# Kernel optimization log

Measured on AMD Instinct MI355X. Metric: run time of the kernel, lower is better.

Reference implementation:

```python
import jax, jax.numpy as jnp
import numpy as np

N_NODES = 100000
N_EDGES = 3200000
N_GRAPHS = 1000


def gcn_conv(x, row, col, norm, W, b, num_nodes):
    # x: [N, F_in] -> [N, F_out]; PyG GCNConv: linear, then normalized scatter-add
    h = x @ W                                   # [N, F_out]
    msg = norm[:, None] * h[row]                # gather from source nodes
    out = jax.ops.segment_sum(msg, col, num_segments=num_nodes)  # scatter to targets
    return out + b


def gcn_norm(edge_index, edge_weight, num_nodes):
    # add self-loops with weight 1.0 (PyG default, improved=False)
    loops = jnp.arange(num_nodes, dtype=edge_index.dtype)
    row = jnp.concatenate([edge_index[0], loops])
    col = jnp.concatenate([edge_index[1], loops])
    w = jnp.concatenate([edge_weight, jnp.ones(num_nodes, edge_weight.dtype)])
    deg = jax.ops.segment_sum(w, col, num_segments=num_nodes)
    dinv = jnp.where(deg > 0, jax.lax.rsqrt(jnp.maximum(deg, 1e-30)), 0.0)
    norm = dinv[row] * w * dinv[col]
    return row, col, norm


def setup_inputs() -> dict:
    key = jax.random.key(0)
    ks = jax.random.split(key, 8)
    x = jax.random.normal(ks[0], (N_NODES, 3), dtype=jnp.float32)
    edge_index = jax.random.randint(ks[1], (2, N_EDGES), 0, N_NODES, dtype=jnp.int64)
    edge_weight = jax.random.uniform(ks[2], (N_EDGES,), dtype=jnp.float32)
    batch = jnp.sort(jax.random.randint(ks[3], (N_NODES,), 0, N_GRAPHS, dtype=jnp.int64))
    W1 = jax.random.normal(ks[4], (3, 16), dtype=jnp.float32) * (1.0 / np.sqrt(3))
    b1 = jnp.zeros((16,), jnp.float32)
    W2 = jax.random.normal(ks[5], (16, 16), dtype=jnp.float32) * 0.25
    b2 = jnp.zeros((16,), jnp.float32)
    Wlin = jax.random.normal(ks[6], (16, 7), dtype=jnp.float32) * 0.25
    blin = jnp.zeros((7,), jnp.float32)
    return {"x": x, "edge_index": edge_index, "edge_weight": edge_weight,
            "batch": batch, "W1": W1, "b1": b1, "W2": W2, "b2": b2,
            "Wlin": Wlin, "blin": blin}


def reference(x, edge_index, edge_weight, batch, W1, b1, W2, b2, Wlin, blin):
    num_nodes = x.shape[0]
    row, col, norm = gcn_norm(edge_index, edge_weight, num_nodes)
    h = jax.nn.relu(gcn_conv(x, row, col, norm, W1, b1, num_nodes))
    h = jax.nn.relu(gcn_conv(h, row, col, norm, W2, b2, num_nodes))
    pooled = jax.ops.segment_sum(h, batch, num_segments=N_GRAPHS)  # [G, 16]
    return pooled @ Wlin + blin  # [G, 7]
```

## Files before the change

### kernel.cpp

```cpp
#include <hip/hip_runtime.h>


#define SH 6
#define RB 64
#define KMAX 2048
#define KST (KMAX + 1)
#define TPB 256
#define BCAP 8192
#define PT 1024
#define PB 256
#define NP 4
#define ETCAP 12800

typedef unsigned short ushort_t;
typedef unsigned char u8;
typedef unsigned long long u64;

__device__ __forceinline__ ushort_t f2bf(float v) {
    unsigned u = __float_as_uint(v);
    u += 0x7FFFu + ((u >> 16) & 1u);
    return (ushort_t)(u >> 16);
}

__device__ __forceinline__ unsigned quantw(float w) {
    unsigned wq = (unsigned)__float2int_rn(w * 32768.0f);
    return wq > 32767u ? 32767u : wq;
}

__global__ __launch_bounds__(PT)
void k_part(const int* __restrict__ row, const int* __restrict__ col,
            const float* __restrict__ ew, unsigned* __restrict__ bcnt,
            unsigned* __restrict__ bof, uint2* __restrict__ brc,
            int E, int K, int tile, int KP) {
    __shared__ unsigned lh[KMAX];
    __shared__ unsigned cur[KMAX];
    __shared__ unsigned wt[PT / 64];
    __shared__ unsigned lc[ETCAP];
    __shared__ unsigned lp[ETCAP];
    int tid = threadIdx.x, b = blockIdx.x;
    int e0 = min(b * tile, E), e1 = min(b * tile + tile, E);
    int cnt = e1 - e0;
    unsigned base = (unsigned)e0;
    bool staged = (cnt <= ETCAP);
    for (int i = tid; i < KMAX; i += PT) lh[i] = 0u;
    __syncthreads();
    if (staged) {
        for (int j = tid; j < cnt; j += PT) {
            int e = e0 + j;
            int c = col[e];
            lc[j] = (unsigned)c;
            lp[j] = (unsigned)row[e] | (quantw(ew[e]) << 17);
            atomicAdd(&lh[c >> SH], 1u);
        }
    } else {
        for (int e = e0 + tid; e < e1; e += PT) atomicAdd(&lh[col[e] >> SH], 1u);
    }
    __syncthreads();
    for (int i = tid; i < K; i += PT) {
        unsigned c = lh[i];
        if (c) atomicAdd(&bcnt[i], c);
    }
    int i0 = tid << 1;
    unsigned a0 = lh[i0], a1 = lh[i0 + 1];
    unsigned ts = a0 + a1, v = ts;
#pragma unroll
    for (int o = 1; o < 64; o <<= 1) {
        unsigned u = __shfl_up(v, o, 64);
        if ((tid & 63) >= o) v += u;
    }
    if ((tid & 63) == 63) wt[tid >> 6] = v;
    __syncthreads();
    if (tid == 0) {
        unsigned acc = 0;
#pragma unroll
        for (int w = 0; w < PT / 64; w++) { unsigned t = wt[w]; wt[w] = acc; acc += t; }
    }
    __syncthreads();
    unsigned ex = wt[tid >> 6] + (v - ts);
    unsigned* bo = bof + (size_t)b * KST;
    cur[i0] = base + ex;          bo[i0] = base + ex;
    cur[i0 + 1] = base + ex + a0; bo[i0 + 1] = base + ex + a0;
    if (tid == PT - 1) bo[KMAX] = base + ex + ts;
    __syncthreads();
    for (int p = 0; p < NP; ++p) {
        int lo = p * KP, hi = min(lo + KP, K);
        if (staged) {
            for (int j = tid; j < cnt; j += PT) {
                unsigned c = lc[j];
                int bkt = (int)(c >> SH);
                if (bkt >= lo && bkt < hi) {
                    unsigned pos = atomicAdd(&cur[bkt], 1u);
                    brc[pos] = make_uint2(lp[j], c);
                }
            }
        } else {
            for (int e = e0 + tid; e < e1; e += PT) {
                int c = col[e];
                int bkt = c >> SH;
                if (bkt >= lo && bkt < hi) {
                    unsigned pos = atomicAdd(&cur[bkt], 1u);
                    brc[pos] = make_uint2((unsigned)row[e] | (quantw(ew[e]) << 17),
                                          (unsigned)c);
                }
            }
        }
        __syncthreads();
    }
}

__global__ void k_scan(const unsigned* __restrict__ cnt, unsigned* __restrict__ start,
                       int K) {
    __shared__ unsigned a[KMAX], b[KMAX];
    int t = threadIdx.x;
    for (int i = t; i < KMAX; i += 1024) a[i] = (i < K) ? cnt[i] : 0u;
    __syncthreads();
    unsigned *src = a, *dst = b;
    for (int off = 1; off < KMAX; off <<= 1) {
        for (int i = t; i < KMAX; i += 1024)
            dst[i] = (i >= off) ? src[i] + src[i - off] : src[i];
        __syncthreads();
        unsigned* tmp = src; src = dst; dst = tmp;
    }
    for (int i = t; i < K; i += 1024) start[i] = (i == 0) ? 0u : src[i - 1];
}

__global__ __launch_bounds__(TPB)
void k_grp(const uint2* __restrict__ brc, const unsigned* __restrict__ bof,
           const unsigned* __restrict__ bst, const float* __restrict__ x,
           const float* __restrict__ W1, unsigned* __restrict__ srt,
           unsigned* __restrict__ cptr, float* __restrict__ dinv,
           unsigned* __restrict__ g1b, float* __restrict__ acc1,
           int N, int E, int K) {
    int orig = blockIdx.x;
    int q8 = K >> 3, r8 = K & 7;
    int xcd = orig & 7, idx = orig >> 3;
    int k = (xcd < r8 ? xcd * (q8 + 1) : r8 * (q8 + 1) + (xcd - r8) * q8) + idx;
    int node0 = k << SH;

    __shared__ unsigned ebuf[BCAP];
    __shared__ u8 cbuf[BCAP];
    __shared__ u8 seg[BCAP];
    __shared__ unsigned rsrc[PB];
    __shared__ unsigned roff[PB + 1];
    __shared__ unsigned wt4[TPB / 64];
    __shared__ unsigned cnt64[RB], st64[RB], dq[RB];
    __shared__ float dl[RB], lx[RB * 3], lw[48];
    int tid = threadIdx.x;
    unsigned s = bst[k];
    if (tid < RB) { cnt64[tid] = 0u; dq[tid] = 0u; }
    if (tid < 48) lw[tid] = W1[tid];
    int nn = min(RB, N - node0);
    for (int i = tid; i < nn * 3; i += TPB) lx[i] = x[(size_t)node0 * 3 + i];

    unsigned rl;
    {
        unsigned s0 = bof[(size_t)tid * KST + k];
        unsigned s1 = bof[(size_t)tid * KST + k + 1];
        rsrc[tid] = s0;
        rl = s1 - s0;
    }
    unsigned v = rl;
#pragma unroll
    for (int o = 1; o < 64; o <<= 1) {
        unsigned u = __shfl_up(v, o, 64);
        if ((tid & 63) >= o) v += u;
    }
    if ((tid & 63) == 63) wt4[tid >> 6] = v;
    __syncthreads();
    if (tid == 0) {
        unsigned acc = 0;
#pragma unroll
        for (int w = 0; w < TPB / 64; w++) { unsigned t = wt4[w]; wt4[w] = acc; acc += t; }
    }
    __syncthreads();
    unsigned ex = wt4[tid >> 6] + (v - rl);
    roff[tid] = ex;
    if (tid == PB - 1) roff[PB] = ex + rl;
    __syncthreads();
    unsigned c = roff[PB];

    bool fits = (c <= (unsigned)BCAP);
    if (fits) {
        for (unsigned j = ex; j < ex + rl; ++j) seg[j] = (u8)tid;
        __syncthreads();
        for (unsigned j = tid; j < c; j += TPB) {
            unsigned r = seg[j];
            unsigned src = rsrc[r] + (j - roff[r]);
            uint2 p = brc[src];
            unsigned cl = p.y & 63u;
            ebuf[j] = p.x; cbuf[j] = (u8)cl;
            atomicAdd(&cnt64[cl], 1u);
            atomicAdd(&dq[cl], p.x >> 17);
        }
        __syncthreads();
        if (tid == 0) {
            unsigned acc = 0;
            for (int i = 0; i < RB; i++) { st64[i] = acc; acc += cnt64[i]; cnt64[i] = 0u; }
        }
        __syncthreads();
        for (unsigned j = tid; j < c; j += TPB) {
            unsigned cl = cbuf[j];
            unsigned pos = st64[cl] + atomicAdd(&cnt64[cl], 1u);
            srt[s + pos] = ebuf[j];
        }
    } else {
#define MAP_SRC(j, srcv)                                                       \
        {                                                                      \
            int lo = 0, hi = PB - 1;                                           \
            _Pragma("unroll")                                                  \
            for (int it = 0; it < 8; ++it) {                                   \
                int mid = (lo + hi + 1) >> 1;                                  \
                if (roff[mid] <= (j)) lo = mid; else hi = mid - 1;             \
            }                                                                  \
            (srcv) = rsrc[lo] + ((j) - roff[lo]);                              \
        }
        for (unsigned j = tid; j < c; j += TPB) {
            unsigned src; MAP_SRC(j, src);
            uint2 p = brc[src];
            unsigned cl = p.y & 63u;
            atomicAdd(&cnt64[cl], 1u);
            atomicAdd(&dq[cl], p.x >> 17);
        }
        __syncthreads();
        if (tid == 0) {
            unsigned acc = 0;
            for (int i = 0; i < RB; i++) { st64[i] = acc; acc += cnt64[i]; cnt64[i] = 0u; }
        }
        __syncthreads();
        for (unsigned j = tid; j < c; j += TPB) {
            unsigned src; MAP_SRC(j, src);
            uint2 p = brc[src];
            unsigned cl = p.y & 63u;
            unsigned pos = st64[cl] + atomicAdd(&cnt64[cl], 1u);
            srt[s + pos] = p.x;
        }
#undef MAP_SRC
    }
    __syncthreads();
    if (tid < RB) {
        float d = rsqrtf(1.0f + (float)dq[tid] * (1.0f / 32768.0f));
        dl[tid] = d;
        if (tid < nn) {
            dinv[node0 + tid] = d;
            cptr[node0 + tid] = s + st64[tid];
        }
    }
    if (tid == 0 && node0 + nn == N) cptr[N] = (unsigned)E;
    __syncthreads();
    float* gtmp = (float*)ebuf;
    for (int idx2 = tid; idx2 < nn * 16; idx2 += TPB) {
        int n = idx2 >> 4, f = idx2 & 15;
        float vv = dl[n] * (lx[n * 3] * lw[f] + lx[n * 3 + 1] * lw[16 + f] +
                            lx[n * 3 + 2] * lw[32 + f]);
        acc1[(size_t)(node0 + n) * 16 + f] = vv;
        gtmp[idx2] = vv;
    }
    __syncthreads();
    for (int idx2 = tid; idx2 < nn * 8; idx2 += TPB) {
        int n = idx2 >> 3, qq = idx2 & 7;
        g1b[(size_t)(node0 + n) * 8 + qq] =
            (unsigned)f2bf(gtmp[n * 16 + 2 * qq]) |
            ((unsigned)f2bf(gtmp[n * 16 + 2 * qq + 1]) << 16);
    }
}

__global__ __launch_bounds__(TPB)
void k_csr(const unsigned* __restrict__ srt, const unsigned* __restrict__ cptr,
           const unsigned* __restrict__ gb, float* __restrict__ acc, int N) {
    int t = blockIdx.x * TPB + threadIdx.x;
    int c = t >> 3, f2 = t & 7;
    if (c >= N) return;
    unsigned e = cptr[c], end = cptr[c + 1];
    float a = 0.0f, b = 0.0f;
#pragma unroll 4
    for (; e < end; ++e) {
        unsigned m = srt[e];
        float w = (float)(m >> 17) * (1.0f / 32768.0f);
        unsigned u = gb[(size_t)(m & 0x1FFFFu) * 8 + f2];
        a = fmaf(w, __uint_as_float(u << 16), a);
        b = fmaf(w, __uint_as_float(u & 0xFFFF0000u), b);
    }
    float2* p = (float2*)&acc[(size_t)c * 16 + 2 * f2];
    float2 v = *p;
    v.x += a; v.y += b;
    *p = v;
}

__global__ void k_mid(const float* __restrict__ acc1, const float* __restrict__ dinv,
                      const float* __restrict__ b1, const float* __restrict__ W2,
                      unsigned* __restrict__ g2b, float* __restrict__ acc2, int N) {
    __shared__ float t[16][16];
    __shared__ float go[16][16];
    __shared__ float w2[256];
    int tid = threadIdx.x;
    int il = tid >> 4, f = tid & 15;
    int i = blockIdx.x * 16 + il;
    w2[tid] = W2[tid];
    float v = 0.0f, d = 0.0f;
    if (i < N) {
        d = dinv[i];
        v = b1[f] + d * acc1[(size_t)i * 16 + f];
        v = v > 0.0f ? v : 0.0f;
    }
    t[il][f] = v;
    __syncthreads();
    float r = 0.0f;
    if (i < N) {
        float o = 0.0f;
#pragma unroll
        for (int kk = 0; kk < 16; kk++) o += t[il][kk] * w2[kk * 16 + f];
        r = d * o;
        acc2[(size_t)i * 16 + f] = r;
    }
    go[il][f] = r;
    __syncthreads();
    if (tid < 128) {
        int il2 = tid >> 3, q = tid & 7;
        int i2 = blockIdx.x * 16 + il2;
        if (i2 < N)
            g2b[(size_t)i2 * 8 + q] = (unsigned)f2bf(go[il2][2 * q]) |
                                      ((unsigned)f2bf(go[il2][2 * q + 1]) << 16);
    }
}

#define PC 1024
__global__ void k_pool(const float* __restrict__ acc2, const float* __restrict__ dinv,
                       const float* __restrict__ b2, const int* __restrict__ batch,
                       float* __restrict__ pooled, int N, int G) {
    int b0 = blockIdx.x * PC;
    int nodes = min(PC, N - b0);
    __shared__ float lacc[64 * 16];
    __shared__ int lbat[PC];
    int tid = threadIdx.x;
    for (int i = tid; i < nodes; i += 256) lbat[i] = batch[b0 + i];
    __syncthreads();
    int gmin = lbat[0], gmax = lbat[nodes - 1];
    bool fits = (gmax - gmin < 64);
    if (fits) {
        for (int i = tid; i < 64 * 16; i += 256) lacc[i] = 0.0f;
        __syncthreads();
    }
    for (int idx = tid; idx < nodes * 16; idx += 256) {
        int i = idx >> 4, f = idx & 15;
        int n = b0 + i;
        float d = dinv[n];
        float v = b2[f] + d * acc2[(size_t)n * 16 + f];
        v = v > 0.0f ? v : 0.0f;
        if (fits) atomicAdd(&lacc[(lbat[i] - gmin) * 16 + f], v);
        else      atomicAdd(&pooled[lbat[i] * 16 + f], v);
    }
    if (fits) {
        __syncthreads();
        for (int idx = tid; idx < 64 * 16; idx += 256) {
            int g = gmin + (idx >> 4);
            float v = lacc[idx];
            if (g < G && v != 0.0f) atomicAdd(&pooled[g * 16 + (idx & 15)], v);
        }
    }
}

__global__ void k_final(const float* __restrict__ pooled, const float* __restrict__ Wlin,
                        const float* __restrict__ blin, float* __restrict__ out, int G) {
    int t = blockIdx.x * blockDim.x + threadIdx.x;
    int g = t / 7, j = t % 7;
    if (g >= G) return;
    float v = blin[j];
#pragma unroll
    for (int f = 0; f < 16; f++) v += pooled[g * 16 + f] * Wlin[f * 7 + j];
    out[g * 7 + j] = v;
}

static inline int cdiv_i(long long a, long long b) { return (int)((a + b - 1) / b); }

extern "C" void kernel_launch(void* const* d_in, const int* in_sizes, int n_in,
                              void* d_out, int out_size, void* d_ws, size_t ws_size,
                              hipStream_t stream) {
    const float* x     = (const float*)d_in[0];
    const int*   ei    = (const int*)d_in[1];
    const float* ew    = (const float*)d_in[2];
    const int*   batch = (const int*)d_in[3];
    const float* W1    = (const float*)d_in[4];
    const float* b1    = (const float*)d_in[5];
    const float* W2    = (const float*)d_in[6];
    const float* b2    = (const float*)d_in[7];
    const float* Wlin  = (const float*)d_in[8];
    const float* blin  = (const float*)d_in[9];
    float* out = (float*)d_out;

    const int N = in_sizes[0] / 3;
    const int E = in_sizes[2];
    const int G = out_size / 7;
    const int K = (N + RB - 1) >> SH;
    const int tile = cdiv_i(E, PB);
    const int KP = cdiv_i(K, NP);
    const int* row = ei;
    const int* col = ei + E;

    uint2*    brc    = (uint2*)d_ws;
    unsigned* srt    = (unsigned*)(brc + E);
    float*    dinv   = (float*)(srt + E);
    unsigned* g1b    = (unsigned*)(dinv + N);
    unsigned* g2b    = g1b + (size_t)N * 8;
    float*    acc1   = (float*)(g2b + (size_t)N * 8);
    float*    acc2   = acc1 + (size_t)N * 16;
    unsigned* cptr   = (unsigned*)(acc2 + (size_t)N * 16);
    unsigned* bst    = cptr + N + 1;
    unsigned* bof    = bst + KMAX;
    unsigned* bcnt   = bof + (size_t)PB * KST;
    float*    pooled = (float*)(bcnt + KMAX);

    hipMemsetAsync(bcnt, 0, (KMAX + (size_t)G * 16) * sizeof(unsigned), stream);

    k_part<<<PB, PT, 0, stream>>>(row, col, ew, bcnt, bof, brc, E, K, tile, KP);
    k_scan<<<1, 1024, 0, stream>>>(bcnt, bst, K);
    k_grp<<<K, TPB, 0, stream>>>(brc, bof, bst, x, W1, srt, cptr, dinv, g1b, acc1,
                                 N, E, K);

    k_csr<<<cdiv_i((long long)N * 8, TPB), TPB, 0, stream>>>(srt, cptr, g1b, acc1, N);

    k_mid<<<cdiv_i(N, 16), TPB, 0, stream>>>(acc1, dinv, b1, W2, g2b, acc2, N);

    k_csr<<<cdiv_i((long long)N * 8, TPB), TPB, 0, stream>>>(srt, cptr, g2b, acc2, N);

    k_pool<<<cdiv_i(N, PC), TPB, 0, stream>>>(acc2, dinv, b2, batch, pooled, N, G);
    k_final<<<cdiv_i((long long)G * 7, TPB), TPB, 0, stream>>>(pooled, Wlin, blin, out, G);
}
```

Before: 252.4 us.

## Fuse layer-1 epilogue and W2 transform into CSR gather, widen per-thread features

The mid-layer kernel (bias, ReLU, 16x16 W2 matmul, bf16 packing) is folded into the first CSR aggregation kernel. Each node's row is now computed with wave shuffles across four threads instead of through shared memory. Both CSR kernels now give each thread four features via uint2 gathers rather than two features with 32-bit loads. This removes one launch and the round trip of acc1 through global memory, and halves the threads and index loads per edge, at the cost of fewer threads for hiding gather latency.

```diff
diff --git a/kernel.cpp b/kernel.cpp
--- a/kernel.cpp
+++ b/kernel.cpp
@@ -265,62 +265,73 @@
 }
 
 __global__ __launch_bounds__(TPB)
-void k_csr(const unsigned* __restrict__ srt, const unsigned* __restrict__ cptr,
-           const unsigned* __restrict__ gb, float* __restrict__ acc, int N) {
+void k_csr1(const unsigned* __restrict__ srt, const unsigned* __restrict__ cptr,
+            const uint2* __restrict__ gb2, const float* __restrict__ acc1,
+            const float* __restrict__ dinv, const float* __restrict__ b1,
+            const float* __restrict__ W2, unsigned* __restrict__ g2b,
+            float* __restrict__ acc2, int N) {
     int t = blockIdx.x * TPB + threadIdx.x;
-    int c = t >> 3, f2 = t & 7;
+    int c = t >> 2, f4 = t & 3;
     if (c >= N) return;
     unsigned e = cptr[c], end = cptr[c + 1];
-    float a = 0.0f, b = 0.0f;
+    float s0 = 0.0f, s1 = 0.0f, s2 = 0.0f, s3 = 0.0f;
 #pragma unroll 4
     for (; e < end; ++e) {
         unsigned m = srt[e];
         float w = (float)(m >> 17) * (1.0f / 32768.0f);
-        unsigned u = gb[(size_t)(m & 0x1FFFFu) * 8 + f2];
-        a = fmaf(w, __uint_as_float(u << 16), a);
-        b = fmaf(w, __uint_as_float(u & 0xFFFF0000u), b);
-    }
-    float2* p = (float2*)&acc[(size_t)c * 16 + 2 * f2];
-    float2 v = *p;
-    v.x += a; v.y += b;
+        uint2 u = gb2[(size_t)(m & 0x1FFFFu) * 4 + f4];
+        s0 = fmaf(w, __uint_as_float(u.x << 16), s0);
+        s1 = fmaf(w, __uint_as_float(u.x & 0xFFFF0000u), s1);
+        s2 = fmaf(w, __uint_as_float(u.y << 16), s2);
+        s3 = fmaf(w, __uint_as_float(u.y & 0xFFFF0000u), s3);
+    }
+    float d = dinv[c];
+    const float4 se = *(const float4*)&acc1[(size_t)c * 16 + 4 * f4];
+    const float4 bb = *(const float4*)&b1[4 * f4];
+    float h[4];
+    h[0] = fmaxf(bb.x + d * (se.x + s0), 0.0f);
+    h[1] = fmaxf(bb.y + d * (se.y + s1), 0.0f);
+    h[2] = fmaxf(bb.z + d * (se.z + s2), 0.0f);
+    h[3] = fmaxf(bb.w + d * (se.w + s3), 0.0f);
+    int base = (threadIdx.x & 63) & ~3;
+    float o0 = 0.0f, o1 = 0.0f, o2 = 0.0f, o3 = 0.0f;
+#pragma unroll
+    for (int kk = 0; kk < 16; ++kk) {
+        float hk = __shfl(h[kk & 3], base + (kk >> 2), 64);
+        const float4 wv = *(const float4*)&W2[kk * 16 + 4 * f4];
+        o0 = fmaf(hk, wv.x, o0);
+        o1 = fmaf(hk, wv.y, o1);
+        o2 = fmaf(hk, wv.z, o2);
+        o3 = fmaf(hk, wv.w, o3);
+    }
+    float r0 = d * o0, r1 = d * o1, r2 = d * o2, r3 = d * o3;
+    *(float4*)&acc2[(size_t)c * 16 + 4 * f4] = make_float4(r0, r1, r2, r3);
+    g2b[(size_t)c * 8 + 2 * f4]     = (unsigned)f2bf(r0) | ((unsigned)f2bf(r1) << 16);
+    g2b[(size_t)c * 8 + 2 * f4 + 1] = (unsigned)f2bf(r2) | ((unsigned)f2bf(r3) << 16);
+}
+
+__global__ __launch_bounds__(TPB)
+void k_csr2(const unsigned* __restrict__ srt, const unsigned* __restrict__ cptr,
+            const uint2* __restrict__ gb2, float* __restrict__ acc, int N) {
+    int t = blockIdx.x * TPB + threadIdx.x;
+    int c = t >> 2, f4 = t & 3;
+    if (c >= N) return;
+    unsigned e = cptr[c], end = cptr[c + 1];
+    float s0 = 0.0f, s1 = 0.0f, s2 = 0.0f, s3 = 0.0f;
+#pragma unroll 4
+    for (; e < end; ++e) {
+        unsigned m = srt[e];
+        float w = (float)(m >> 17) * (1.0f / 32768.0f);
+        uint2 u = gb2[(size_t)(m & 0x1FFFFu) * 4 + f4];
+        s0 = fmaf(w, __uint_as_float(u.x << 16), s0);
+        s1 = fmaf(w, __uint_as_float(u.x & 0xFFFF0000u), s1);
+        s2 = fmaf(w, __uint_as_float(u.y << 16), s2);
+        s3 = fmaf(w, __uint_as_float(u.y & 0xFFFF0000u), s3);
+    }
+    float4* p = (float4*)&acc[(size_t)c * 16 + 4 * f4];
+    float4 v = *p;
+    v.x += s0; v.y += s1; v.z += s2; v.w += s3;
     *p = v;
-}
-
-__global__ void k_mid(const float* __restrict__ acc1, const float* __restrict__ dinv,
-                      const float* __restrict__ b1, const float* __restrict__ W2,
-                      unsigned* __restrict__ g2b, float* __restrict__ acc2, int N) {
-    __shared__ float t[16][16];
-    __shared__ float go[16][16];
-    __shared__ float w2[256];
-    int tid = threadIdx.x;
-    int il = tid >> 4, f = tid & 15;
-    int i = blockIdx.x * 16 + il;
-    w2[tid] = W2[tid];
-    float v = 0.0f, d = 0.0f;
-    if (i < N) {
-        d = dinv[i];
-        v = b1[f] + d * acc1[(size_t)i * 16 + f];
-        v = v > 0.0f ? v : 0.0f;
-    }
-    t[il][f] = v;
-    __syncthreads();
-    float r = 0.0f;
-    if (i < N) {
-        float o = 0.0f;
-#pragma unroll
-        for (int kk = 0; kk < 16; kk++) o += t[il][kk] * w2[kk * 16 + f];
-        r = d * o;
-        acc2[(size_t)i * 16 + f] = r;
-    }
-    go[il][f] = r;
-    __syncthreads();
-    if (tid < 128) {
-        int il2 = tid >> 3, q = tid & 7;
-        int i2 = blockIdx.x * 16 + il2;
-        if (i2 < N)
-            g2b[(size_t)i2 * 8 + q] = (unsigned)f2bf(go[il2][2 * q]) |
-                                      ((unsigned)f2bf(go[il2][2 * q + 1]) << 16);
-    }
 }
 
 #define PC 1024
@@ -416,11 +427,11 @@
     k_grp<<<K, TPB, 0, stream>>>(brc, bof, bst, x, W1, srt, cptr, dinv, g1b, acc1,
                                  N, E, K);
 
-    k_csr<<<cdiv_i((long long)N * 8, TPB), TPB, 0, stream>>>(srt, cptr, g1b, acc1, N);
-
-    k_mid<<<cdiv_i(N, 16), TPB, 0, stream>>>(acc1, dinv, b1, W2, g2b, acc2, N);
-
-    k_csr<<<cdiv_i((long long)N * 8, TPB), TPB, 0, stream>>>(srt, cptr, g2b, acc2, N);
+    k_csr1<<<cdiv_i((long long)N * 4, TPB), TPB, 0, stream>>>(
+        srt, cptr, (const uint2*)g1b, acc1, dinv, b1, W2, g2b, acc2, N);
+
+    k_csr2<<<cdiv_i((long long)N * 4, TPB), TPB, 0, stream>>>(
+        srt, cptr, (const uint2*)g2b, acc2, N);
 
     k_pool<<<cdiv_i(N, PC), TPB, 0, stream>>>(acc2, dinv, b2, batch, pooled, N, G);
     k_final<<<cdiv_i((long long)G * 7, TPB), TPB, 0, stream>>>(pooled, Wlin, blin, out, G);
```

Measured after the change: 250.5 us. About the same (-0.8%).
